# Kernel tuning notes

Measured on AMD Instinct MI355X. Metric: run time of the kernel, lower is better.

The kernel has to match this reference:

```python
import jax, jax.numpy as jnp
import numpy as np

THRESHOLD = 0.004  # graph_threshold from init_kwargs
EPS = 1e-12


def setup_inputs() -> dict:
    key = jax.random.key(0)
    kf, kw = jax.random.split(key)
    features = jax.random.normal(kf, (8192, 128), dtype=jnp.float32)
    weight = jax.random.normal(kw, (128, 128), dtype=jnp.float32)
    return {"features": features, "weight": weight}


def reference(features, weight):
    # Pairwise state fidelity: squared dot product of row-normalized vectors.
    n = features.shape[0]
    xn = features / (jnp.linalg.norm(features, axis=1, keepdims=True) + EPS)
    fid = (xn @ xn.T) ** 2  # [N, N]
    # Edge weight 1.0 where fid >= threshold (secondary=None); no self-loops.
    adj = (fid >= THRESHOLD).astype(features.dtype)
    adj = adj * (1.0 - jnp.eye(n, dtype=features.dtype))
    aggregated = adj @ features  # [N, F]
    # relu(W @ agg.T).T == relu(agg @ W.T)
    return jax.nn.relu(aggregated @ weight.T)
```

## Files before the change

### kernel.cpp

```cpp
#include <hip/hip_runtime.h>
#include <math.h>

#define NROWS  8192
#define NF     128
#define THRF   0.004f
#define BM     64
#define BN     64
#define HALF_N 4096
#define NITER  64

typedef _Float16 f16;
typedef __attribute__((ext_vector_type(8))) _Float16 f16x8;
typedef __attribute__((ext_vector_type(4))) float f32x4;

#define MFMA16F(a, b, c) __builtin_amdgcn_mfma_f32_16x16x32_f16(a, b, c, 0, 0, 0)

#define RH_OFF 0
#define RL_OFF 32768
#define TB_OFF 65536
#define PB_OFF 98304
#define IJ_OFF 106496
#define SM_BYTES 107008

typedef __attribute__((address_space(1))) const unsigned int g_u32;
typedef __attribute__((address_space(3))) unsigned int l_u32;

__device__ __forceinline__ void gload16(const void* g, void* l) {
    __builtin_amdgcn_global_load_lds((g_u32*)g, (l_u32*)l, 16, 0, 0);
}

__device__ __forceinline__ unsigned short f16bits(f16 x) {
    return __builtin_bit_cast(unsigned short, x);
}

__global__ __launch_bounds__(256) void prep_k(const float* __restrict__ X,
                                              float* __restrict__ inv_norm,
                                              unsigned short* __restrict__ Xh,
                                              unsigned short* __restrict__ Xl,
                                              unsigned short* __restrict__ XhT) {
    __shared__ unsigned short sT[64][136];
    const int t  = threadIdx.x;
    const int jb = blockIdx.x * 64;
    const int row = t >> 2, c0 = (t & 3) * 32;
    const int grow = jb + row;

    float v[32];
    {
        const float* src = X + (size_t)grow * NF + c0;
        #pragma unroll
        for (int k = 0; k < 8; ++k) {
            f32x4 e = *reinterpret_cast<const f32x4*>(src + 4 * k);
            v[4 * k]     = e[0]; v[4 * k + 1] = e[1];
            v[4 * k + 2] = e[2]; v[4 * k + 3] = e[3];
        }
    }
    float ss = 0.f;
    #pragma unroll
    for (int k = 0; k < 32; ++k) ss += v[k] * v[k];
    ss += __shfl_xor(ss, 1);
    ss += __shfl_xor(ss, 2);
    if ((t & 3) == 0) inv_norm[grow] = 1.0f / (sqrtf(ss) + 1e-12f);

    #pragma unroll
    for (int k = 0; k < 4; ++k) {
        unsigned hw[4], lw[4];
        #pragma unroll
        for (int p = 0; p < 4; ++p) {
            float a = v[8 * k + 2 * p], b = v[8 * k + 2 * p + 1];
            f16 ha = (f16)a, hb = (f16)b;
            f16 la = (f16)((a - (float)ha) * 2048.0f);
            f16 lb = (f16)((b - (float)hb) * 2048.0f);
            hw[p] = (unsigned)f16bits(ha) | ((unsigned)f16bits(hb) << 16);
            lw[p] = (unsigned)f16bits(la) | ((unsigned)f16bits(lb) << 16);
        }
        uint4 h4 = {hw[0], hw[1], hw[2], hw[3]};
        uint4 l4 = {lw[0], lw[1], lw[2], lw[3]};
        *reinterpret_cast<uint4*>(Xh + (size_t)grow * NF + c0 + 8 * k) = h4;
        *reinterpret_cast<uint4*>(Xl + (size_t)grow * NF + c0 + 8 * k) = l4;
        unsigned* sp = reinterpret_cast<unsigned*>(&sT[row][c0 + 8 * k]);
        sp[0] = hw[0]; sp[1] = hw[1]; sp[2] = hw[2]; sp[3] = hw[3];
    }
    __syncthreads();
    {
        int f = t >> 1, qh = t & 1;
        unsigned um[16];
        #pragma unroll
        for (int m = 0; m < 16; ++m) {
            int j = 32 * qh + 2 * m;
            um[m] = (unsigned)sT[j][f] | ((unsigned)sT[j + 1][f] << 16);
        }
        unsigned* dst = reinterpret_cast<unsigned*>(XhT + (size_t)f * NROWS + jb + 32 * qh);
        #pragma unroll
        for (int m = 0; m < 16; ++m) dst[m] = um[m];
    }
}

__device__ __forceinline__ void issue_tiles(const unsigned short* __restrict__ Xh,
                                            const unsigned short* __restrict__ Xl,
                                            const unsigned short* __restrict__ XhT,
                                            char* SM, int w, int l, int jwin, int buf) {
    const int r16 = l >> 4, c16 = l & 15;
    #pragma unroll
    for (int u = 0; u < 2; ++u) {
        int jloc = 8 * w + 4 * u + r16;
        size_t src = (size_t)(jwin + jloc) * NF + ((c16 ^ (jloc & 15)) << 3);
        char* ldsH = SM + RH_OFF + buf * 16384 + (8 * w + 4 * u) * 256;
        char* ldsL = SM + RL_OFF + buf * 16384 + (8 * w + 4 * u) * 256;
        gload16(Xh + src, ldsH);
        gload16(Xl + src, ldsL);
    }
    const int r8 = l >> 3, c8 = l & 7;
    #pragma unroll
    for (int u = 0; u < 2; ++u) {
        int floc = 16 * w + 8 * u + r8;
        const unsigned short* src = XhT + (size_t)floc * NROWS + jwin + ((c8 ^ (floc & 7)) << 3);
        char* ldsT = SM + TB_OFF + buf * 16384 + (16 * w + 8 * u) * 128;
        gload16(src, ldsT);
    }
}

__global__ __launch_bounds__(512, 1) void fused_k(const unsigned short* __restrict__ Xh,
                                                  const unsigned short* __restrict__ Xl,
                                                  const unsigned short* __restrict__ XhT,
                                                  const float* __restrict__ inv_norm,
                                                  float* __restrict__ pAgg0,
                                                  float* __restrict__ pAgg1) {
    __shared__ __align__(16) char SM[SM_BYTES];
    const int t = threadIdx.x;
    const int w = t >> 6, l = t & 63, l15 = l & 15, h = l >> 4;
    const int im = w >> 2;
    const int jn = w & 3;
    const int bid   = blockIdx.x;
    const int ibase = (bid >> 1) * BM;
    const int qoff  = (bid & 1) * HALF_N;
    float* pAgg = (bid & 1) ? pAgg1 : pAgg0;

    f16x8 aH[8], aL[8];
    #pragma unroll
    for (int ii = 0; ii < 2; ++ii)
        #pragma unroll
        for (int ks = 0; ks < 4; ++ks) {
            size_t ro = (size_t)(ibase + 32 * im + 16 * ii + l15) * NF + 32 * ks + 8 * h;
            aH[ii * 4 + ks] = *reinterpret_cast<const f16x8*>(Xh + ro);
            aL[ii * 4 + ks] = *reinterpret_cast<const f16x8*>(Xl + ro);
        }
    float invI2[8];
    #pragma unroll
    for (int ii = 0; ii < 2; ++ii)
        #pragma unroll
        for (int q = 0; q < 4; ++q) {
            float x = inv_norm[ibase + 32 * im + 16 * ii + 4 * h + q];
            invI2[ii * 4 + q] = x * x;
        }
    const int jl = 16 * jn + l15;

    issue_tiles(Xh, Xl, XhT, SM, w, l, qoff, 0);
    if (t < BN) { float x = inv_norm[qoff + t]; ((float*)(SM + IJ_OFF))[t] = x * x; }

    f32x4 agg00 = {0,0,0,0}, agg01 = {0,0,0,0}, agg10 = {0,0,0,0}, agg11 = {0,0,0,0};

    for (int it = 0; it < NITER; ++it) {
        const int buf  = it & 1;
        const int jwin = qoff + it * BN;
        __syncthreads();
        if (it + 1 < NITER) {
            issue_tiles(Xh, Xl, XhT, SM, w, l, jwin + BN, buf ^ 1);
            if (t < BN) {
                float x = inv_norm[jwin + BN + t];
                ((float*)(SM + IJ_OFF))[(buf ^ 1) * BN + t] = x * x;
            }
        }
        const char* rh = SM + RH_OFF + buf * 16384;
        const char* rl = SM + RL_OFF + buf * 16384;
        f32x4 Shi0 = {0,0,0,0}, Shi1 = {0,0,0,0};
        f32x4 SA0  = {0,0,0,0}, SA1  = {0,0,0,0};
        f32x4 SB0  = {0,0,0,0}, SB1  = {0,0,0,0};
        __builtin_amdgcn_s_setprio(1);
        #pragma unroll
        for (int ks = 0; ks < 4; ++ks) {
            int boff = jl * 256 + (((4 * ks + h) ^ (jl & 15)) << 4);
            f16x8 bh = *reinterpret_cast<const f16x8*>(rh + boff);
            f16x8 bl = *reinterpret_cast<const f16x8*>(rl + boff);
            Shi0 = MFMA16F(aH[ks],     bh, Shi0);
            Shi1 = MFMA16F(aH[4 + ks], bh, Shi1);
            SA0  = MFMA16F(aH[ks],     bl, SA0);
            SA1  = MFMA16F(aH[4 + ks], bl, SA1);
            SB0  = MFMA16F(aL[ks],     bh, SB0);
            SB1  = MFMA16F(aL[4 + ks], bh, SB1);
        }
        __builtin_amdgcn_s_setprio(0);
        {
            float ij2v = ((const float*)(SM + IJ_OFF))[buf * BN + jl];
            int ecmp = (jwin + jl) - (ibase + 32 * im + 4 * h);
            #pragma unroll
            for (int q = 0; q < 4; ++q) {
                float vv = Shi0[q] + (SA0[q] + SB0[q]) * (1.0f / 2048.0f);
                float t2 = vv * vv * invI2[q] * ij2v;
                bool p = (t2 >= THRF) && (ecmp != q);
                int il = 32 * im + 4 * h + q;
                int pb = il * 128 + ((jl * 2) ^ ((il & 7) << 4));
                *reinterpret_cast<unsigned short*>(SM + PB_OFF + pb) =
                    p ? (unsigned short)0x3C00 : (unsigned short)0;
            }
            #pragma unroll
            for (int q = 0; q < 4; ++q) {
                float vv = Shi1[q] + (SA1[q] + SB1[q]) * (1.0f / 2048.0f);
                float t2 = vv * vv * invI2[4 + q] * ij2v;
                bool p = (t2 >= THRF) && (ecmp != 16 + q);
                int il = 32 * im + 16 + 4 * h + q;
                int pb = il * 128 + ((jl * 2) ^ ((il & 7) << 4));
                *reinterpret_cast<unsigned short*>(SM + PB_OFF + pb) =
                    p ? (unsigned short)0x3C00 : (unsigned short)0;
            }
        }
        asm volatile("s_waitcnt lgkmcnt(0)\n\ts_barrier" ::: "memory");
        const char* tbp = SM + TB_OFF + buf * 16384;
        __builtin_amdgcn_s_setprio(1);
        #pragma unroll
        for (int kj = 0; kj < 2; ++kj) {
            int il0 = 32 * im + l15, il1 = il0 + 16;
            f16x8 pa0 = *reinterpret_cast<const f16x8*>(
                SM + PB_OFF + il0 * 128 + ((64 * kj + 16 * h) ^ ((il0 & 7) << 4)));
            f16x8 pa1 = *reinterpret_cast<const f16x8*>(
                SM + PB_OFF + il1 * 128 + ((64 * kj + 16 * h) ^ ((il1 & 7) << 4)));
            int f0 = 32 * jn + l15, f1 = f0 + 16;
            f16x8 bt0 = *reinterpret_cast<const f16x8*>(
                tbp + f0 * 128 + ((64 * kj + 16 * h) ^ ((f0 & 7) << 4)));
            f16x8 bt1 = *reinterpret_cast<const f16x8*>(
                tbp + f1 * 128 + ((64 * kj + 16 * h) ^ ((f1 & 7) << 4)));
            agg00 = MFMA16F(pa0, bt0, agg00);
            agg01 = MFMA16F(pa0, bt1, agg01);
            agg10 = MFMA16F(pa1, bt0, agg10);
            agg11 = MFMA16F(pa1, bt1, agg11);
        }
        __builtin_amdgcn_s_setprio(0);
    }
    #pragma unroll
    for (int q = 0; q < 4; ++q) {
        int r0 = ibase + 32 * im + 4 * h + q;
        int r1 = r0 + 16;
        int c0 = 32 * jn + l15, c1 = c0 + 16;
        pAgg[(size_t)r0 * NF + c0] = agg00[q];
        pAgg[(size_t)r0 * NF + c1] = agg01[q];
        pAgg[(size_t)r1 * NF + c0] = agg10[q];
        pAgg[(size_t)r1 * NF + c1] = agg11[q];
    }
}

__global__ __launch_bounds__(256) void combine_k(const float* __restrict__ pAgg1,
                                                 const float* __restrict__ Wm,
                                                 float* __restrict__ out) {
    __shared__ float sW[NF * NF];
    __shared__ float sSum[32][132];
    const int t = threadIdx.x;
    const size_t base = (size_t)blockIdx.x * 32 * NF;
    #pragma unroll
    for (int k = 0; k < 16; ++k) {
        int u4 = t + 256 * k;
        reinterpret_cast<f32x4*>(sW)[u4] = reinterpret_cast<const f32x4*>(Wm)[u4];
    }
    #pragma unroll
    for (int k = 0; k < 16; ++k) {
        int u = t + 256 * k;
        float v = out[base + u] + pAgg1[base + u];
        sSum[u >> 7][u & 127] = v;
    }
    __syncthreads();
    const int r = t & 31, og = t >> 5;
    float acc[16];
    #pragma unroll
    for (int oi = 0; oi < 16; ++oi) acc[oi] = 0.f;
    #pragma unroll 8
    for (int k4 = 0; k4 < 32; ++k4) {
        f32x4 a4 = *reinterpret_cast<const f32x4*>(&sSum[r][4 * k4]);
        #pragma unroll
        for (int oi = 0; oi < 16; ++oi) {
            f32x4 w4 = *reinterpret_cast<const f32x4*>(&sW[(og * 16 + oi) * NF + 4 * k4]);
            acc[oi] += a4[0] * w4[0] + a4[1] * w4[1] + a4[2] * w4[2] + a4[3] * w4[3];
        }
    }
    #pragma unroll
    for (int o4 = 0; o4 < 4; ++o4) {
        f32x4 v4;
        #pragma unroll
        for (int e = 0; e < 4; ++e) {
            float v = acc[o4 * 4 + e];
            v4[e] = v > 0.f ? v : 0.f;
        }
        *reinterpret_cast<f32x4*>(out + base + r * NF + og * 16 + o4 * 4) = v4;
    }
}

extern "C" void kernel_launch(void* const* d_in, const int* in_sizes, int n_in,
                              void* d_out, int out_size, void* d_ws, size_t ws_size,
                              hipStream_t stream) {
    const float* feat = (const float*)d_in[0];
    const float* Wm   = (const float*)d_in[1];
    float* out        = (float*)d_out;

    char* ws = (char*)d_ws;
    unsigned short* Xh  = (unsigned short*)(ws);
    unsigned short* Xl  = (unsigned short*)(ws + (2u << 20));
    unsigned short* XhT = (unsigned short*)(ws + (4u << 20));
    float* inv_norm     = (float*)(ws + (6u << 20));
    float* pAgg1        = (float*)(ws + (6u << 20) + 32768);

    prep_k<<<NROWS / 64, 256, 0, stream>>>(feat, inv_norm, Xh, Xl, XhT);
    fused_k<<<256, 512, 0, stream>>>(Xh, Xl, XhT, inv_norm, out, pAgg1);
    combine_k<<<NROWS / 32, 256, 0, stream>>>(pAgg1, Wm, out);
}
```

Baseline: 116.5 us.

## Halve row tile, read low-part B from global, store second partial as fp16

Halves the row tile from 64 to 32, which doubles the grid to 512 blocks. The low-half B operand now comes straight from global memory instead of LDS, cutting shared memory use to about 70KB. Together with launch bounds allowing multiple blocks per CU, this aims for more occupancy and better parallelism. The second partial aggregate is written in fp16 to cut traffic in the combine step, which adds rounding risk on integer-valued sums of features.

```diff
diff --git a/kernel.cpp b/kernel.cpp
--- a/kernel.cpp
+++ b/kernel.cpp
@@ -1,26 +1,26 @@
 #include <hip/hip_runtime.h>
 #include <math.h>
 
-#define NROWS  8192
-#define NF     128
-#define THRF   0.004f
-#define BM     64
-#define BN     64
-#define HALF_N 4096
-#define NITER  64
+#define NROWS 8192
+#define NF    128
+#define THRF  0.004f
+#define BM    32
+#define BN    64
+#define QN    4096
+#define NITER 64
 
 typedef _Float16 f16;
 typedef __attribute__((ext_vector_type(8))) _Float16 f16x8;
+typedef __attribute__((ext_vector_type(4))) _Float16 f16x4;
 typedef __attribute__((ext_vector_type(4))) float f32x4;
 
 #define MFMA16F(a, b, c) __builtin_amdgcn_mfma_f32_16x16x32_f16(a, b, c, 0, 0, 0)
 
 #define RH_OFF 0
-#define RL_OFF 32768
-#define TB_OFF 65536
-#define PB_OFF 98304
-#define IJ_OFF 106496
-#define SM_BYTES 107008
+#define TB_OFF 32768
+#define PB_OFF 65536
+#define IJ_OFF 69632
+#define SM_BYTES 70144
 
 typedef __attribute__((address_space(1))) const unsigned int g_u32;
 typedef __attribute__((address_space(3))) unsigned int l_u32;
@@ -96,7 +96,6 @@
 }
 
 __device__ __forceinline__ void issue_tiles(const unsigned short* __restrict__ Xh,
-                                            const unsigned short* __restrict__ Xl,
                                             const unsigned short* __restrict__ XhT,
                                             char* SM, int w, int l, int jwin, int buf) {
     const int r16 = l >> 4, c16 = l & 15;
@@ -104,27 +103,23 @@
     for (int u = 0; u < 2; ++u) {
         int jloc = 8 * w + 4 * u + r16;
         size_t src = (size_t)(jwin + jloc) * NF + ((c16 ^ (jloc & 15)) << 3);
-        char* ldsH = SM + RH_OFF + buf * 16384 + (8 * w + 4 * u) * 256;
-        char* ldsL = SM + RL_OFF + buf * 16384 + (8 * w + 4 * u) * 256;
-        gload16(Xh + src, ldsH);
-        gload16(Xl + src, ldsL);
+        gload16(Xh + src, SM + RH_OFF + buf * 16384 + (8 * w + 4 * u) * 256);
     }
     const int r8 = l >> 3, c8 = l & 7;
     #pragma unroll
     for (int u = 0; u < 2; ++u) {
         int floc = 16 * w + 8 * u + r8;
         const unsigned short* src = XhT + (size_t)floc * NROWS + jwin + ((c8 ^ (floc & 7)) << 3);
-        char* ldsT = SM + TB_OFF + buf * 16384 + (16 * w + 8 * u) * 128;
-        gload16(src, ldsT);
-    }
-}
-
-__global__ __launch_bounds__(512, 1) void fused_k(const unsigned short* __restrict__ Xh,
+        gload16(src, SM + TB_OFF + buf * 16384 + (16 * w + 8 * u) * 128);
+    }
+}
+
+__global__ __launch_bounds__(512, 4) void fused_k(const unsigned short* __restrict__ Xh,
                                                   const unsigned short* __restrict__ Xl,
                                                   const unsigned short* __restrict__ XhT,
                                                   const float* __restrict__ inv_norm,
-                                                  float* __restrict__ pAgg0,
-                                                  float* __restrict__ pAgg1) {
+                                                  float* __restrict__ out,
+                                                  _Float16* __restrict__ p1) {
     __shared__ __align__(16) char SM[SM_BYTES];
     const int t = threadIdx.x;
     const int w = t >> 6, l = t & 63, l15 = l & 15, h = l >> 4;
@@ -132,122 +127,112 @@
     const int jn = w & 3;
     const int bid   = blockIdx.x;
     const int ibase = (bid >> 1) * BM;
-    const int qoff  = (bid & 1) * HALF_N;
-    float* pAgg = (bid & 1) ? pAgg1 : pAgg0;
-
-    f16x8 aH[8], aL[8];
-    #pragma unroll
-    for (int ii = 0; ii < 2; ++ii)
+    const int qq    = bid & 1;
+    const int qbase = qq * QN;
+
+    f16x8 aH[4], aL[4];
+    {
+        const size_t ro = (size_t)(ibase + 16 * im + l15) * NF;
         #pragma unroll
         for (int ks = 0; ks < 4; ++ks) {
-            size_t ro = (size_t)(ibase + 32 * im + 16 * ii + l15) * NF + 32 * ks + 8 * h;
-            aH[ii * 4 + ks] = *reinterpret_cast<const f16x8*>(Xh + ro);
-            aL[ii * 4 + ks] = *reinterpret_cast<const f16x8*>(Xl + ro);
-        }
-    float invI2[8];
-    #pragma unroll
-    for (int ii = 0; ii < 2; ++ii)
-        #pragma unroll
-        for (int q = 0; q < 4; ++q) {
-            float x = inv_norm[ibase + 32 * im + 16 * ii + 4 * h + q];
-            invI2[ii * 4 + q] = x * x;
-        }
+            aH[ks] = *reinterpret_cast<const f16x8*>(Xh + ro + 32 * ks + 8 * h);
+            aL[ks] = *reinterpret_cast<const f16x8*>(Xl + ro + 32 * ks + 8 * h);
+        }
+    }
+    float invI2[4];
+    #pragma unroll
+    for (int q = 0; q < 4; ++q) {
+        float x = inv_norm[ibase + 16 * im + 4 * h + q];
+        invI2[q] = x * x;
+    }
     const int jl = 16 * jn + l15;
 
-    issue_tiles(Xh, Xl, XhT, SM, w, l, qoff, 0);
-    if (t < BN) { float x = inv_norm[qoff + t]; ((float*)(SM + IJ_OFF))[t] = x * x; }
-
-    f32x4 agg00 = {0,0,0,0}, agg01 = {0,0,0,0}, agg10 = {0,0,0,0}, agg11 = {0,0,0,0};
+    issue_tiles(Xh, XhT, SM, w, l, qbase, 0);
+    if (t < BN) { float x = inv_norm[qbase + t]; ((float*)(SM + IJ_OFF))[t] = x * x; }
+
+    f32x4 agg0 = {0,0,0,0}, agg1 = {0,0,0,0};
 
     for (int it = 0; it < NITER; ++it) {
         const int buf  = it & 1;
-        const int jwin = qoff + it * BN;
+        const int jwin = qbase + it * BN;
         __syncthreads();
         if (it + 1 < NITER) {
-            issue_tiles(Xh, Xl, XhT, SM, w, l, jwin + BN, buf ^ 1);
+            issue_tiles(Xh, XhT, SM, w, l, jwin + BN, buf ^ 1);
             if (t < BN) {
                 float x = inv_norm[jwin + BN + t];
                 ((float*)(SM + IJ_OFF))[(buf ^ 1) * BN + t] = x * x;
             }
         }
+        f16x8 blg[4];
+        {
+            const unsigned short* xlr = Xl + (size_t)(jwin + jl) * NF + 8 * h;
+            #pragma unroll
+            for (int ks = 0; ks < 4; ++ks)
+                blg[ks] = *reinterpret_cast<const f16x8*>(xlr + 32 * ks);
+        }
+        float ij2 = ((const float*)(SM + IJ_OFF))[buf * BN + jl];
+
         const char* rh = SM + RH_OFF + buf * 16384;
-        const char* rl = SM + RL_OFF + buf * 16384;
-        f32x4 Shi0 = {0,0,0,0}, Shi1 = {0,0,0,0};
-        f32x4 SA0  = {0,0,0,0}, SA1  = {0,0,0,0};
-        f32x4 SB0  = {0,0,0,0}, SB1  = {0,0,0,0};
+        f32x4 Shi = {0,0,0,0}, Slo = {0,0,0,0};
         __builtin_amdgcn_s_setprio(1);
         #pragma unroll
         for (int ks = 0; ks < 4; ++ks) {
             int boff = jl * 256 + (((4 * ks + h) ^ (jl & 15)) << 4);
             f16x8 bh = *reinterpret_cast<const f16x8*>(rh + boff);
-            f16x8 bl = *reinterpret_cast<const f16x8*>(rl + boff);
-            Shi0 = MFMA16F(aH[ks],     bh, Shi0);
-            Shi1 = MFMA16F(aH[4 + ks], bh, Shi1);
-            SA0  = MFMA16F(aH[ks],     bl, SA0);
-            SA1  = MFMA16F(aH[4 + ks], bl, SA1);
-            SB0  = MFMA16F(aL[ks],     bh, SB0);
-            SB1  = MFMA16F(aL[4 + ks], bh, SB1);
+            Shi = MFMA16F(aH[ks], bh,      Shi);
+            Slo = MFMA16F(aL[ks], bh,      Slo);
+            Slo = MFMA16F(aH[ks], blg[ks], Slo);
         }
         __builtin_amdgcn_s_setprio(0);
+
         {
-            float ij2v = ((const float*)(SM + IJ_OFF))[buf * BN + jl];
-            int ecmp = (jwin + jl) - (ibase + 32 * im + 4 * h);
+            int ecmp = (jwin + jl) - (ibase + 16 * im + 4 * h);
             #pragma unroll
             for (int q = 0; q < 4; ++q) {
-                float vv = Shi0[q] + (SA0[q] + SB0[q]) * (1.0f / 2048.0f);
-                float t2 = vv * vv * invI2[q] * ij2v;
+                float vv = Shi[q] + Slo[q] * (1.0f / 2048.0f);
+                float t2 = vv * vv * invI2[q] * ij2;
                 bool p = (t2 >= THRF) && (ecmp != q);
-                int il = 32 * im + 4 * h + q;
+                int il = 16 * im + 4 * h + q;
                 int pb = il * 128 + ((jl * 2) ^ ((il & 7) << 4));
                 *reinterpret_cast<unsigned short*>(SM + PB_OFF + pb) =
                     p ? (unsigned short)0x3C00 : (unsigned short)0;
             }
-            #pragma unroll
-            for (int q = 0; q < 4; ++q) {
-                float vv = Shi1[q] + (SA1[q] + SB1[q]) * (1.0f / 2048.0f);
-                float t2 = vv * vv * invI2[4 + q] * ij2v;
-                bool p = (t2 >= THRF) && (ecmp != 16 + q);
-                int il = 32 * im + 16 + 4 * h + q;
-                int pb = il * 128 + ((jl * 2) ^ ((il & 7) << 4));
-                *reinterpret_cast<unsigned short*>(SM + PB_OFF + pb) =
-                    p ? (unsigned short)0x3C00 : (unsigned short)0;
-            }
         }
         asm volatile("s_waitcnt lgkmcnt(0)\n\ts_barrier" ::: "memory");
+
         const char* tbp = SM + TB_OFF + buf * 16384;
         __builtin_amdgcn_s_setprio(1);
         #pragma unroll
         for (int kj = 0; kj < 2; ++kj) {
-            int il0 = 32 * im + l15, il1 = il0 + 16;
-            f16x8 pa0 = *reinterpret_cast<const f16x8*>(
-                SM + PB_OFF + il0 * 128 + ((64 * kj + 16 * h) ^ ((il0 & 7) << 4)));
-            f16x8 pa1 = *reinterpret_cast<const f16x8*>(
-                SM + PB_OFF + il1 * 128 + ((64 * kj + 16 * h) ^ ((il1 & 7) << 4)));
+            int ir = 16 * im + l15;
+            f16x8 pa = *reinterpret_cast<const f16x8*>(
+                SM + PB_OFF + ir * 128 + ((64 * kj + 16 * h) ^ ((ir & 7) << 4)));
             int f0 = 32 * jn + l15, f1 = f0 + 16;
             f16x8 bt0 = *reinterpret_cast<const f16x8*>(
                 tbp + f0 * 128 + ((64 * kj + 16 * h) ^ ((f0 & 7) << 4)));
             f16x8 bt1 = *reinterpret_cast<const f16x8*>(
                 tbp + f1 * 128 + ((64 * kj + 16 * h) ^ ((f1 & 7) << 4)));
-            agg00 = MFMA16F(pa0, bt0, agg00);
-            agg01 = MFMA16F(pa0, bt1, agg01);
-            agg10 = MFMA16F(pa1, bt0, agg10);
-            agg11 = MFMA16F(pa1, bt1, agg11);
+            agg0 = MFMA16F(pa, bt0, agg0);
+            agg1 = MFMA16F(pa, bt1, agg1);
         }
         __builtin_amdgcn_s_setprio(0);
     }
+
     #pragma unroll
     for (int q = 0; q < 4; ++q) {
-        int r0 = ibase + 32 * im + 4 * h + q;
-        int r1 = r0 + 16;
+        int row = ibase + 16 * im + 4 * h + q;
         int c0 = 32 * jn + l15, c1 = c0 + 16;
-        pAgg[(size_t)r0 * NF + c0] = agg00[q];
-        pAgg[(size_t)r0 * NF + c1] = agg01[q];
-        pAgg[(size_t)r1 * NF + c0] = agg10[q];
-        pAgg[(size_t)r1 * NF + c1] = agg11[q];
-    }
-}
-
-__global__ __launch_bounds__(256) void combine_k(const float* __restrict__ pAgg1,
+        if (qq == 0) {
+            out[(size_t)row * NF + c0] = agg0[q];
+            out[(size_t)row * NF + c1] = agg1[q];
+        } else {
+            p1[(size_t)row * NF + c0] = (_Float16)agg0[q];
+            p1[(size_t)row * NF + c1] = (_Float16)agg1[q];
+        }
+    }
+}
+
+__global__ __launch_bounds__(256) void combine_k(const _Float16* __restrict__ p1,
                                                  const float* __restrict__ Wm,
                                                  float* __restrict__ out) {
     __shared__ float sW[NF * NF];
@@ -260,10 +245,13 @@
         reinterpret_cast<f32x4*>(sW)[u4] = reinterpret_cast<const f32x4*>(Wm)[u4];
     }
     #pragma unroll
-    for (int k = 0; k < 16; ++k) {
-        int u = t + 256 * k;
-        float v = out[base + u] + pAgg1[base + u];
-        sSum[u >> 7][u & 127] = v;
+    for (int k = 0; k < 4; ++k) {
+        int u4 = t + 256 * k;
+        f32x4 v = reinterpret_cast<const f32x4*>(out + base)[u4];
+        f16x4 a = reinterpret_cast<const f16x4*>(p1 + base)[u4];
+        #pragma unroll
+        for (int e = 0; e < 4; ++e) v[e] += (float)a[e];
+        *reinterpret_cast<f32x4*>(&sSum[u4 >> 5][(4 * u4) & 127]) = v;
     }
     __syncthreads();
     const int r = t & 31, og = t >> 5;
@@ -303,9 +291,9 @@
     unsigned short* Xl  = (unsigned short*)(ws + (2u << 20));
     unsigned short* XhT = (unsigned short*)(ws + (4u << 20));
     float* inv_norm     = (float*)(ws + (6u << 20));
-    float* pAgg1        = (float*)(ws + (6u << 20) + 32768);
+    _Float16* p1        = (_Float16*)(ws + (6u << 20) + 32768);
 
     prep_k<<<NROWS / 64, 256, 0, stream>>>(feat, inv_norm, Xh, Xl, XhT);
-    fused_k<<<256, 512, 0, stream>>>(Xh, Xl, XhT, inv_norm, out, pAgg1);
-    combine_k<<<NROWS / 32, 256, 0, stream>>>(pAgg1, Wm, out);
-}
+    fused_k<<<512, 512, 0, stream>>>(Xh, Xl, XhT, inv_norm, out, p1);
+    combine_k<<<NROWS / 32, 256, 0, stream>>>(p1, Wm, out);
+}
```

Result: slower. 178.3 us (+53.0%).
